# Optimization experiments

Measured on AMD Instinct MI355X. Metric: run time of the kernel, lower is better.

The kernel has to match this reference:

```python
import jax, jax.numpy as jnp
import numpy as np

N_NODES = 50000
N_EDGES = 800000
D = 64
N_GRAPHS = 512
N_LAYERS = 3
HID_FC = 64
N_CLASSES = 10


def setup_inputs() -> dict:
    key = jax.random.key(0)
    ks = jax.random.split(key, 12)
    s = 1.0 / np.sqrt(D)
    x = jax.random.normal(ks[0], (N_NODES, D), dtype=jnp.float32)
    edge_index = jax.random.randint(ks[1], (2, N_EDGES), 0, N_NODES, dtype=jnp.int32)
    batch = jnp.sort(jax.random.randint(ks[2], (N_NODES,), 0, N_GRAPHS, dtype=jnp.int32))
    convW1 = jax.random.normal(ks[3], (N_LAYERS, D, D), dtype=jnp.float32) * s
    convb1 = jax.random.normal(ks[4], (N_LAYERS, D), dtype=jnp.float32) * 0.01
    convW2 = jax.random.normal(ks[5], (N_LAYERS, D, D), dtype=jnp.float32) * s
    convb2 = jax.random.normal(ks[6], (N_LAYERS, D), dtype=jnp.float32) * 0.01
    fcW1 = jax.random.normal(ks[7], (D, HID_FC), dtype=jnp.float32) * s
    fcb1 = jax.random.normal(ks[8], (HID_FC,), dtype=jnp.float32) * 0.01
    fcW2 = jax.random.normal(ks[9], (HID_FC, N_CLASSES), dtype=jnp.float32) * (1.0 / np.sqrt(HID_FC))
    fcb2 = jax.random.normal(ks[10], (N_CLASSES,), dtype=jnp.float32) * 0.01
    return {"x": x, "convW1": convW1, "convb1": convb1, "convW2": convW2,
            "convb2": convb2, "fcW1": fcW1, "fcb1": fcb1, "fcW2": fcW2,
            "fcb2": fcb2, "edge_index": edge_index, "batch": batch}


def reference(x, convW1, convb1, convW2, convb2, fcW1, fcb1, fcW2, fcb2, edge_index, batch):
    src, dst = edge_index[0], edge_index[1]
    h = x
    for l in range(N_LAYERS):
        # GIN aggregation: (1 + eps) * x + sum_{j in N(i)} x_j, eps = 0
        agg = jax.ops.segment_sum(h[src], dst, num_segments=N_NODES)
        h = h + agg
        # per-layer MLP: Linear -> ReLU -> Linear
        h = jax.nn.relu(h @ convW1[l] + convb1[l])
        h = h @ convW2[l] + convb2[l]
    # global max pool over nodes of each graph
    g = jax.ops.segment_max(h, batch, num_segments=N_GRAPHS)
    # FC head: Linear(64) -> ReLU -> Linear(num_classes)
    g = jax.nn.relu(g @ fcW1 + fcb1)
    logits = g @ fcW2 + fcb2
    return jax.nn.log_softmax(logits, axis=1)
```

## Files before the change

kernel.cpp:

```cpp
#include <hip/hip_runtime.h>
#include <math.h>

#define N_NODES 50000
#define N_EDGES 800000
#define D 64
#define N_GRAPHS 512
#define N_CLASSES 10
#define NT 3125
#define NPART 6250

#define SCAN_B 512
#define NB_SCAN ((N_NODES + SCAN_B - 1) / SCAN_B)

typedef __attribute__((ext_vector_type(8))) short bf16x8;
typedef __attribute__((ext_vector_type(4))) float f32x4;

#define MFMA16(a, b, c) __builtin_amdgcn_mfma_f32_16x16x32_bf16(a, b, c, 0, 0, 0)


__device__ __forceinline__ unsigned mapf(float f) {
  unsigned u = __float_as_uint(f);
  return (u & 0x80000000u) ? ~u : (u | 0x80000000u);
}
__device__ __forceinline__ float unmapf(unsigned u) {
  return __uint_as_float((u & 0x80000000u) ? (u & 0x7FFFFFFFu) : ~u);
}
__device__ __forceinline__ ushort bf16_rne(float f) {
  unsigned u = __float_as_uint(f);
  u += 0x7FFFu + ((u >> 16) & 1u);
  return (ushort)(u >> 16);
}
__device__ __forceinline__ float bf16_tof(ushort h) {
  return __uint_as_float(((unsigned)h) << 16);
}
__device__ __forceinline__ unsigned pack2(float a, float b) {
  return (unsigned)bf16_rne(a) | ((unsigned)bf16_rne(b) << 16);
}
__device__ __forceinline__ float2 unpack2(unsigned v) {
  return make_float2(__uint_as_float(v << 16), __uint_as_float(v & 0xFFFF0000u));
}


__global__ void to_bf16(const float* __restrict__ in, unsigned* __restrict__ out) {
  int i = blockIdx.x * 256 + threadIdx.x;
  float4 v = reinterpret_cast<const float4*>(in)[i];
  reinterpret_cast<uint2*>(out)[i] = make_uint2(pack2(v.x, v.y), pack2(v.z, v.w));
}


__global__ void wprep(const float* __restrict__ convW1, const float* __restrict__ convW2,
                      ushort* __restrict__ wf) {
  const int wi = blockIdx.x;
  const int layer = wi >> 1, which = wi & 1;
  const float* W = (which ? convW2 : convW1) + layer * 4096;
  const int t = threadIdx.x;
  const int f = t >> 6, lane = t & 63;
  const int ct = f >> 1, ks = f & 1;
  const int n = ct * 16 + (lane & 15);
  const int k0 = ks * 32 + ((lane >> 4) << 3);
  ushort hi[8], lo[8];
#pragma unroll
  for (int v = 0; v < 8; ++v) {
    float w = W[(k0 + v) * 64 + n];
    ushort h = bf16_rne(w);
    hi[v] = h;
    lo[v] = bf16_rne(w - bf16_tof(h));
  }
  ushort* base = wf + layer * 16384 + which * 8192;
  *(uint4*)(base + f * 512 + lane * 8) = *(uint4*)hi;
  *(uint4*)(base + 4096 + f * 512 + lane * 8) = *(uint4*)lo;
}


__global__ void hist_part(const int* __restrict__ dst, int* __restrict__ deg) {
  const int p = blockIdx.x & 7;
  const int lo = p * NPART, hi = lo + NPART;
  const int stride = (gridDim.x >> 3) * 256;
  for (int e = (blockIdx.x >> 3) * 256 + threadIdx.x; e < N_EDGES; e += stride) {
    int d = dst[e];
    if (d >= lo && d < hi) atomicAdd(&deg[d], 1);
  }
}

__global__ void scan_blocks(const int* __restrict__ deg, int* __restrict__ bsum) {
  __shared__ int sd[SCAN_B];
  int i = blockIdx.x * SCAN_B + threadIdx.x;
  sd[threadIdx.x] = (i < N_NODES) ? deg[i] : 0;
  __syncthreads();
  for (int off = SCAN_B / 2; off > 0; off >>= 1) {
    if (threadIdx.x < off) sd[threadIdx.x] += sd[threadIdx.x + off];
    __syncthreads();
  }
  if (threadIdx.x == 0) bsum[blockIdx.x] = sd[0];
}

__global__ void scan_mid(int* __restrict__ bsum) {
  __shared__ int s[256];
  int t = threadIdx.x;
  if (t < NB_SCAN) s[t] = bsum[t];
  __syncthreads();
  if (t == 0) {
    int run = 0;
    for (int i = 0; i < NB_SCAN; ++i) { int v = s[i]; s[i] = run; run += v; }
  }
  __syncthreads();
  if (t < NB_SCAN) bsum[t] = s[t];
}

__global__ void scan_final(const int* __restrict__ deg, const int* __restrict__ bsum,
                           int* __restrict__ rs, int* __restrict__ cur) {
  __shared__ int sd[SCAN_B];
  int i = blockIdx.x * SCAN_B + threadIdx.x;
  int v = (i < N_NODES) ? deg[i] : 0;
  sd[threadIdx.x] = v;
  __syncthreads();
  for (int off = 1; off < SCAN_B; off <<= 1) {
    int add = (threadIdx.x >= off) ? sd[threadIdx.x - off] : 0;
    __syncthreads();
    sd[threadIdx.x] += add;
    __syncthreads();
  }
  if (i < N_NODES) {
    int ex = bsum[blockIdx.x] + sd[threadIdx.x] - v;
    rs[i] = ex;
    cur[i] = ex;
  }
  if (i == 0) rs[N_NODES] = N_EDGES;
}

__global__ void fill_part(const int* __restrict__ src, const int* __restrict__ dst,
                          int* __restrict__ cur, int* __restrict__ csr) {
  const int p = blockIdx.x & 7;
  const int lo = p * NPART, hi = lo + NPART;
  const int stride = (gridDim.x >> 3) * 256;
  for (int e = (blockIdx.x >> 3) * 256 + threadIdx.x; e < N_EDGES; e += stride) {
    int d = dst[e];
    if (d >= lo && d < hi) {
      int pos = atomicAdd(&cur[d], 1);
      csr[pos] = src[e];
    }
  }
}


__global__ __launch_bounds__(256) void agg_bf16(
    const unsigned* __restrict__ hin, const int* __restrict__ csr,
    const int* __restrict__ rs, unsigned* __restrict__ hout) {
  const int t = threadIdx.x;
  const int hw = t >> 5, hl = t & 31;
  const int node = blockIdx.x * 8 + hw;
  float2 a = unpack2(hin[node * 32 + hl]);
  int e = rs[node];
  const int e1 = rs[node + 1];
  for (; e + 4 <= e1; e += 4) {
    int s0 = csr[e], s1 = csr[e + 1], s2 = csr[e + 2], s3 = csr[e + 3];
    float2 v0 = unpack2(hin[s0 * 32 + hl]);
    float2 v1 = unpack2(hin[s1 * 32 + hl]);
    float2 v2 = unpack2(hin[s2 * 32 + hl]);
    float2 v3 = unpack2(hin[s3 * 32 + hl]);
    a.x += v0.x + v1.x; a.y += v0.y + v1.y;
    a.x += v2.x + v3.x; a.y += v2.y + v3.y;
  }
  for (; e < e1; ++e) {
    float2 v = unpack2(hin[csr[e] * 32 + hl]);
    a.x += v.x; a.y += v.y;
  }
  hout[node * 32 + hl] = pack2(a.x, a.y);
}


template <int FINAL>
__global__ __launch_bounds__(256, 2) void mlp_bf16(
    const unsigned* __restrict__ Ain,
    unsigned* __restrict__ Aout,
    const ushort* __restrict__ wfL,
    const float* __restrict__ b1, const float* __restrict__ b2,
    const int* __restrict__ batch, unsigned* __restrict__ gU) {
  __shared__ ushort Wl[16384];
  __shared__ ushort tb[4][16 * 72];
  const int t = threadIdx.x;
  const int w = t >> 6, lane = t & 63;
  const int tile = blockIdx.x * 4 + w;
  const bool act = (tile < NT);
  const int m = lane & 15, g = lane >> 4;
  ushort* tw = tb[w];

  {
    const uint4* s = (const uint4*)wfL;
    uint4* d = (uint4*)Wl;
#pragma unroll
    for (int i = 0; i < 8; ++i) d[t + 256 * i] = s[t + 256 * i];
  }

  bf16x8 a0 = {}, a1 = {};
  if (act) {
    const ushort* Ar = (const ushort*)Ain + (size_t)(tile * 16 + m) * 64;
    a0 = *(const bf16x8*)(Ar + g * 8);
    a1 = *(const bf16x8*)(Ar + 32 + g * 8);
  }
  __syncthreads();

  const char* wb = (const char*)Wl + lane * 16;
#define LDW(off) (*(const bf16x8*)(wb + (off)))

  if (act) {
    f32x4 c0 = {0.f, 0.f, 0.f, 0.f}, c1 = c0, c2 = c0, c3 = c0;
#define G1(ct, cc)                                        \
    cc = MFMA16(a0, LDW((2 * ct + 0) * 1024), cc);        \
    cc = MFMA16(a1, LDW((2 * ct + 1) * 1024), cc);        \
    cc = MFMA16(a0, LDW(8192 + (2 * ct + 0) * 1024), cc); \
    cc = MFMA16(a1, LDW(8192 + (2 * ct + 1) * 1024), cc);
    G1(0, c0) G1(1, c1) G1(2, c2) G1(3, c3)
#undef G1

    float bv0 = b1[m], bv1 = b1[16 + m], bv2 = b1[32 + m], bv3 = b1[48 + m];
#define WRT(cc, ct, bv)                                                     \
    tw[(g * 4 + 0) * 72 + ct * 16 + m] = bf16_rne(fmaxf(cc[0] + bv, 0.f));  \
    tw[(g * 4 + 1) * 72 + ct * 16 + m] = bf16_rne(fmaxf(cc[1] + bv, 0.f));  \
    tw[(g * 4 + 2) * 72 + ct * 16 + m] = bf16_rne(fmaxf(cc[2] + bv, 0.f));  \
    tw[(g * 4 + 3) * 72 + ct * 16 + m] = bf16_rne(fmaxf(cc[3] + bv, 0.f));
    WRT(c0, 0, bv0) WRT(c1, 1, bv1) WRT(c2, 2, bv2) WRT(c3, 3, bv3)
#undef WRT
    bf16x8 h0 = *(const bf16x8*)(tw + m * 72 + g * 8);
    bf16x8 h1 = *(const bf16x8*)(tw + m * 72 + 32 + g * 8);

    c0 = (f32x4){0.f, 0.f, 0.f, 0.f}; c1 = c0; c2 = c0; c3 = c0;
#define G2(ct, cc)                                         \
    cc = MFMA16(h0, LDW(16384 + (2 * ct + 0) * 1024), cc); \
    cc = MFMA16(h1, LDW(16384 + (2 * ct + 1) * 1024), cc); \
    cc = MFMA16(h0, LDW(24576 + (2 * ct + 0) * 1024), cc); \
    cc = MFMA16(h1, LDW(24576 + (2 * ct + 1) * 1024), cc);
    G2(0, c0) G2(1, c1) G2(2, c2) G2(3, c3)
#undef G2
#undef LDW

    float bv20 = b2[m], bv21 = b2[16 + m], bv22 = b2[32 + m], bv23 = b2[48 + m];
    if (FINAL) {
      int b40 = batch[tile * 16 + g * 4 + 0];
      int b41 = batch[tile * 16 + g * 4 + 1];
      int b42 = batch[tile * 16 + g * 4 + 2];
      int b43 = batch[tile * 16 + g * 4 + 3];
#define PM(cc, ct, bv)                                          \
      atomicMax(&gU[b40 * 64 + ct * 16 + m], mapf(cc[0] + bv)); \
      atomicMax(&gU[b41 * 64 + ct * 16 + m], mapf(cc[1] + bv)); \
      atomicMax(&gU[b42 * 64 + ct * 16 + m], mapf(cc[2] + bv)); \
      atomicMax(&gU[b43 * 64 + ct * 16 + m], mapf(cc[3] + bv));
      PM(c0, 0, bv20) PM(c1, 1, bv21) PM(c2, 2, bv22) PM(c3, 3, bv23)
#undef PM
    } else {
#define WRO(cc, ct, bv)                                          \
      tw[(g * 4 + 0) * 72 + ct * 16 + m] = bf16_rne(cc[0] + bv); \
      tw[(g * 4 + 1) * 72 + ct * 16 + m] = bf16_rne(cc[1] + bv); \
      tw[(g * 4 + 2) * 72 + ct * 16 + m] = bf16_rne(cc[2] + bv); \
      tw[(g * 4 + 3) * 72 + ct * 16 + m] = bf16_rne(cc[3] + bv);
      WRO(c0, 0, bv20) WRO(c1, 1, bv21) WRO(c2, 2, bv22) WRO(c3, 3, bv23)
#undef WRO
      const int r = lane >> 2, q = lane & 3;
      uint4 v0 = *(const uint4*)(tw + r * 72 + q * 16);
      uint4 v1 = *(const uint4*)(tw + r * 72 + q * 16 + 8);
      ushort* Ao = (ushort*)Aout + (size_t)tile * 1024;
      *(uint4*)(Ao + lane * 16) = v0;
      *(uint4*)(Ao + lane * 16 + 8) = v1;
    }
  }
}


__global__ void init_g(unsigned* __restrict__ gU) {
  int i = blockIdx.x * blockDim.x + threadIdx.x;
  if (i < N_GRAPHS * D) gU[i] = 0x007FFFFFu;
}

__global__ void head_kernel(const unsigned* __restrict__ gU,
                            const float* __restrict__ fcW1, const float* __restrict__ fcb1,
                            const float* __restrict__ fcW2, const float* __restrict__ fcb2,
                            float* __restrict__ out) {
  __shared__ float gbuf[64];
  __shared__ float hid[64];
  __shared__ float logit[N_CLASSES];
  __shared__ float red[2];
  const int gi = blockIdx.x;
  const int t = threadIdx.x;

  gbuf[t] = unmapf(gU[gi * D + t]);
  __syncthreads();

  float a = fcb1[t];
#pragma unroll
  for (int k = 0; k < 64; ++k) a = fmaf(gbuf[k], fcW1[k * 64 + t], a);
  hid[t] = fmaxf(a, 0.0f);
  __syncthreads();

  if (t < N_CLASSES) {
    float l = fcb2[t];
#pragma unroll
    for (int k = 0; k < 64; ++k) l = fmaf(hid[k], fcW2[k * N_CLASSES + t], l);
    logit[t] = l;
  }
  __syncthreads();

  if (t == 0) {
    float mx = logit[0];
    for (int i = 1; i < N_CLASSES; ++i) mx = fmaxf(mx, logit[i]);
    float s = 0.0f;
    for (int i = 0; i < N_CLASSES; ++i) s += expf(logit[i] - mx);
    red[0] = mx;
    red[1] = logf(s);
  }
  __syncthreads();

  if (t < N_CLASSES) out[gi * N_CLASSES + t] = logit[t] - red[0] - red[1];
}


extern "C" void kernel_launch(void* const* d_in, const int* in_sizes, int n_in,
                              void* d_out, int out_size, void* d_ws, size_t ws_size,
                              hipStream_t stream) {
  const float* x      = (const float*)d_in[0];
  const float* convW1 = (const float*)d_in[1];
  const float* convb1 = (const float*)d_in[2];
  const float* convW2 = (const float*)d_in[3];
  const float* convb2 = (const float*)d_in[4];
  const float* fcW1   = (const float*)d_in[5];
  const float* fcb1   = (const float*)d_in[6];
  const float* fcW2   = (const float*)d_in[7];
  const float* fcb2   = (const float*)d_in[8];
  const int*   edge   = (const int*)d_in[9];
  const int*   batch  = (const int*)d_in[10];
  float* out = (float*)d_out;

  const int* src = edge;
  const int* dst = edge + N_EDGES;

  unsigned* xb  = (unsigned*)d_ws;
  unsigned* hbA = xb + (size_t)N_NODES * 32;
  unsigned* hbB = hbA + (size_t)N_NODES * 32;
  unsigned* gU  = hbB + (size_t)N_NODES * 32;
  int* rs  = (int*)(gU + N_GRAPHS * D);
  int* csr = rs + N_NODES + 1;
  ushort* wf = (ushort*)(csr + N_EDGES);
  int* deg  = (int*)hbB;
  int* cur  = deg + N_NODES;
  int* bsum = cur + N_NODES;

  to_bf16<<<(N_NODES * 16) / 256, 256, 0, stream>>>(x, xb);
  wprep<<<6, 512, 0, stream>>>(convW1, convW2, wf);
  init_g<<<(N_GRAPHS * D + 255) / 256, 256, 0, stream>>>(gU);

  hipMemsetAsync(deg, 0, N_NODES * sizeof(int), stream);
  hist_part<<<2048, 256, 0, stream>>>(dst, deg);
  scan_blocks<<<NB_SCAN, SCAN_B, 0, stream>>>(deg, bsum);
  scan_mid<<<1, 256, 0, stream>>>(bsum);
  scan_final<<<NB_SCAN, SCAN_B, 0, stream>>>(deg, bsum, rs, cur);
  fill_part<<<2048, 256, 0, stream>>>(src, dst, cur, csr);

  const int AGG_B = N_NODES / 8;
  const int MLP_B = (NT + 3) / 4;
  agg_bf16<<<AGG_B, 256, 0, stream>>>(xb, csr, rs, hbA);
  mlp_bf16<0><<<MLP_B, 256, 0, stream>>>(hbA, hbB, wf, convb1, convb2, batch, gU);
  agg_bf16<<<AGG_B, 256, 0, stream>>>(hbB, csr, rs, hbA);
  mlp_bf16<0><<<MLP_B, 256, 0, stream>>>(hbA, xb, wf + 16384, convb1 + 64, convb2 + 64,
                                         batch, gU);
  agg_bf16<<<AGG_B, 256, 0, stream>>>(xb, csr, rs, hbA);
  mlp_bf16<1><<<MLP_B, 256, 0, stream>>>(hbA, nullptr, wf + 32768, convb1 + 128,
                                         convb2 + 128, batch, gU);

  head_kernel<<<N_GRAPHS, 64, 0, stream>>>(gU, fcW1, fcb1, fcW2, fcb2, out);
}
```

Measured before the change: 228.7 us.

## Make MLP kernel persistent with tile prefetch and amortized weight loads

Launches a fixed 196-block grid for the per-layer MLP kernel, where each wave loops over up to four 16-row tiles. Weights and biases are staged once per block, and the next tile's activations are prefetched while the current tile is computed. The LDS staging row stride changes from 72 to 68 elements, which makes the 16-byte LDS reads misaligned and may alter bank behaviour. It trades grid parallelism for less redundant weight staging and more load overlap.

```diff
diff --git a/kernel.cpp b/kernel.cpp
--- a/kernel.cpp
+++ b/kernel.cpp
@@ -8,6 +8,7 @@
 #define N_CLASSES 10
 #define NT 3125
 #define NPART 6250
+#define MLP_BLOCKS 196
 
 #define SCAN_B 512
 #define NB_SCAN ((N_NODES + SCAN_B - 1) / SCAN_B)
@@ -177,11 +178,9 @@
     const float* __restrict__ b1, const float* __restrict__ b2,
     const int* __restrict__ batch, unsigned* __restrict__ gU) {
   __shared__ ushort Wl[16384];
-  __shared__ ushort tb[4][16 * 72];
+  __shared__ ushort tb[4][16 * 68];
   const int t = threadIdx.x;
   const int w = t >> 6, lane = t & 63;
-  const int tile = blockIdx.x * 4 + w;
-  const bool act = (tile < NT);
   const int m = lane & 15, g = lane >> 4;
   ushort* tw = tb[w];
 
@@ -192,6 +191,8 @@
     for (int i = 0; i < 8; ++i) d[t + 256 * i] = s[t + 256 * i];
   }
 
+  int tile = blockIdx.x * 4 + w;
+  bool act = (tile < NT);
   bf16x8 a0 = {}, a1 = {};
   if (act) {
     const ushort* Ar = (const ushort*)Ain + (size_t)(tile * 16 + m) * 64;
@@ -201,68 +202,83 @@
   __syncthreads();
 
   const char* wb = (const char*)Wl + lane * 16;
+  const float bv10 = b1[m], bv11 = b1[16 + m], bv12 = b1[32 + m], bv13 = b1[48 + m];
+  const float bv20 = b2[m], bv21 = b2[16 + m], bv22 = b2[32 + m], bv23 = b2[48 + m];
+
 #define LDW(off) (*(const bf16x8*)(wb + (off)))
 
-  if (act) {
-    f32x4 c0 = {0.f, 0.f, 0.f, 0.f}, c1 = c0, c2 = c0, c3 = c0;
+#pragma unroll
+  for (int it = 0; it < 4; ++it) {
+    const int ntile = tile + 4 * MLP_BLOCKS;
+    const bool nact = (it < 3) && (ntile < NT);
+    bf16x8 na0 = {}, na1 = {};
+    if (nact) {
+      const ushort* Ar = (const ushort*)Ain + (size_t)(ntile * 16 + m) * 64;
+      na0 = *(const bf16x8*)(Ar + g * 8);
+      na1 = *(const bf16x8*)(Ar + 32 + g * 8);
+    }
+
+    if (act) {
+      f32x4 c0 = {0.f, 0.f, 0.f, 0.f}, c1 = c0, c2 = c0, c3 = c0;
 #define G1(ct, cc)                                        \
-    cc = MFMA16(a0, LDW((2 * ct + 0) * 1024), cc);        \
-    cc = MFMA16(a1, LDW((2 * ct + 1) * 1024), cc);        \
-    cc = MFMA16(a0, LDW(8192 + (2 * ct + 0) * 1024), cc); \
-    cc = MFMA16(a1, LDW(8192 + (2 * ct + 1) * 1024), cc);
-    G1(0, c0) G1(1, c1) G1(2, c2) G1(3, c3)
+      cc = MFMA16(a0, LDW((2 * ct + 0) * 1024), cc);      \
+      cc = MFMA16(a1, LDW((2 * ct + 1) * 1024), cc);      \
+      cc = MFMA16(a0, LDW(8192 + (2 * ct + 0) * 1024), cc); \
+      cc = MFMA16(a1, LDW(8192 + (2 * ct + 1) * 1024), cc);
+      G1(0, c0) G1(1, c1) G1(2, c2) G1(3, c3)
 #undef G1
 
-    float bv0 = b1[m], bv1 = b1[16 + m], bv2 = b1[32 + m], bv3 = b1[48 + m];
 #define WRT(cc, ct, bv)                                                     \
-    tw[(g * 4 + 0) * 72 + ct * 16 + m] = bf16_rne(fmaxf(cc[0] + bv, 0.f));  \
-    tw[(g * 4 + 1) * 72 + ct * 16 + m] = bf16_rne(fmaxf(cc[1] + bv, 0.f));  \
-    tw[(g * 4 + 2) * 72 + ct * 16 + m] = bf16_rne(fmaxf(cc[2] + bv, 0.f));  \
-    tw[(g * 4 + 3) * 72 + ct * 16 + m] = bf16_rne(fmaxf(cc[3] + bv, 0.f));
-    WRT(c0, 0, bv0) WRT(c1, 1, bv1) WRT(c2, 2, bv2) WRT(c3, 3, bv3)
+      tw[(g * 4 + 0) * 68 + ct * 16 + m] = bf16_rne(fmaxf(cc[0] + bv, 0.f)); \
+      tw[(g * 4 + 1) * 68 + ct * 16 + m] = bf16_rne(fmaxf(cc[1] + bv, 0.f)); \
+      tw[(g * 4 + 2) * 68 + ct * 16 + m] = bf16_rne(fmaxf(cc[2] + bv, 0.f)); \
+      tw[(g * 4 + 3) * 68 + ct * 16 + m] = bf16_rne(fmaxf(cc[3] + bv, 0.f));
+      WRT(c0, 0, bv10) WRT(c1, 1, bv11) WRT(c2, 2, bv12) WRT(c3, 3, bv13)
 #undef WRT
-    bf16x8 h0 = *(const bf16x8*)(tw + m * 72 + g * 8);
-    bf16x8 h1 = *(const bf16x8*)(tw + m * 72 + 32 + g * 8);
-
-    c0 = (f32x4){0.f, 0.f, 0.f, 0.f}; c1 = c0; c2 = c0; c3 = c0;
+      bf16x8 h0 = *(const bf16x8*)(tw + m * 68 + g * 8);
+      bf16x8 h1 = *(const bf16x8*)(tw + m * 68 + 32 + g * 8);
+
+      c0 = (f32x4){0.f, 0.f, 0.f, 0.f}; c1 = c0; c2 = c0; c3 = c0;
 #define G2(ct, cc)                                         \
-    cc = MFMA16(h0, LDW(16384 + (2 * ct + 0) * 1024), cc); \
-    cc = MFMA16(h1, LDW(16384 + (2 * ct + 1) * 1024), cc); \
-    cc = MFMA16(h0, LDW(24576 + (2 * ct + 0) * 1024), cc); \
-    cc = MFMA16(h1, LDW(24576 + (2 * ct + 1) * 1024), cc);
-    G2(0, c0) G2(1, c1) G2(2, c2) G2(3, c3)
+      cc = MFMA16(h0, LDW(16384 + (2 * ct + 0) * 1024), cc); \
+      cc = MFMA16(h1, LDW(16384 + (2 * ct + 1) * 1024), cc); \
+      cc = MFMA16(h0, LDW(24576 + (2 * ct + 0) * 1024), cc); \
+      cc = MFMA16(h1, LDW(24576 + (2 * ct + 1) * 1024), cc);
+      G2(0, c0) G2(1, c1) G2(2, c2) G2(3, c3)
 #undef G2
+
+      if (FINAL) {
+        int b40 = batch[tile * 16 + g * 4 + 0];
+        int b41 = batch[tile * 16 + g * 4 + 1];
+        int b42 = batch[tile * 16 + g * 4 + 2];
+        int b43 = batch[tile * 16 + g * 4 + 3];
+#define PM(cc, ct, bv)                                          \
+        atomicMax(&gU[b40 * 64 + ct * 16 + m], mapf(cc[0] + bv)); \
+        atomicMax(&gU[b41 * 64 + ct * 16 + m], mapf(cc[1] + bv)); \
+        atomicMax(&gU[b42 * 64 + ct * 16 + m], mapf(cc[2] + bv)); \
+        atomicMax(&gU[b43 * 64 + ct * 16 + m], mapf(cc[3] + bv));
+        PM(c0, 0, bv20) PM(c1, 1, bv21) PM(c2, 2, bv22) PM(c3, 3, bv23)
+#undef PM
+      } else {
+#define WRO(cc, ct, bv)                                          \
+        tw[(g * 4 + 0) * 68 + ct * 16 + m] = bf16_rne(cc[0] + bv); \
+        tw[(g * 4 + 1) * 68 + ct * 16 + m] = bf16_rne(cc[1] + bv); \
+        tw[(g * 4 + 2) * 68 + ct * 16 + m] = bf16_rne(cc[2] + bv); \
+        tw[(g * 4 + 3) * 68 + ct * 16 + m] = bf16_rne(cc[3] + bv);
+        WRO(c0, 0, bv20) WRO(c1, 1, bv21) WRO(c2, 2, bv22) WRO(c3, 3, bv23)
+#undef WRO
+        const int r = lane >> 2, q = lane & 3;
+        uint4 v0 = *(const uint4*)(tw + r * 68 + q * 16);
+        uint4 v1 = *(const uint4*)(tw + r * 68 + q * 16 + 8);
+        ushort* Ao = (ushort*)Aout + (size_t)tile * 1024;
+        *(uint4*)(Ao + lane * 16) = v0;
+        *(uint4*)(Ao + lane * 16 + 8) = v1;
+      }
+    }
+
+    a0 = na0; a1 = na1; tile = ntile; act = nact;
+  }
 #undef LDW
-
-    float bv20 = b2[m], bv21 = b2[16 + m], bv22 = b2[32 + m], bv23 = b2[48 + m];
-    if (FINAL) {
-      int b40 = batch[tile * 16 + g * 4 + 0];
-      int b41 = batch[tile * 16 + g * 4 + 1];
-      int b42 = batch[tile * 16 + g * 4 + 2];
-      int b43 = batch[tile * 16 + g * 4 + 3];
-#define PM(cc, ct, bv)                                          \
-      atomicMax(&gU[b40 * 64 + ct * 16 + m], mapf(cc[0] + bv)); \
-      atomicMax(&gU[b41 * 64 + ct * 16 + m], mapf(cc[1] + bv)); \
-      atomicMax(&gU[b42 * 64 + ct * 16 + m], mapf(cc[2] + bv)); \
-      atomicMax(&gU[b43 * 64 + ct * 16 + m], mapf(cc[3] + bv));
-      PM(c0, 0, bv20) PM(c1, 1, bv21) PM(c2, 2, bv22) PM(c3, 3, bv23)
-#undef PM
-    } else {
-#define WRO(cc, ct, bv)                                          \
-      tw[(g * 4 + 0) * 72 + ct * 16 + m] = bf16_rne(cc[0] + bv); \
-      tw[(g * 4 + 1) * 72 + ct * 16 + m] = bf16_rne(cc[1] + bv); \
-      tw[(g * 4 + 2) * 72 + ct * 16 + m] = bf16_rne(cc[2] + bv); \
-      tw[(g * 4 + 3) * 72 + ct * 16 + m] = bf16_rne(cc[3] + bv);
-      WRO(c0, 0, bv20) WRO(c1, 1, bv21) WRO(c2, 2, bv22) WRO(c3, 3, bv23)
-#undef WRO
-      const int r = lane >> 2, q = lane & 3;
-      uint4 v0 = *(const uint4*)(tw + r * 72 + q * 16);
-      uint4 v1 = *(const uint4*)(tw + r * 72 + q * 16 + 8);
-      ushort* Ao = (ushort*)Aout + (size_t)tile * 1024;
-      *(uint4*)(Ao + lane * 16) = v0;
-      *(uint4*)(Ao + lane * 16 + 8) = v1;
-    }
-  }
 }
 
 
@@ -355,15 +371,14 @@
   fill_part<<<2048, 256, 0, stream>>>(src, dst, cur, csr);
 
   const int AGG_B = N_NODES / 8;
-  const int MLP_B = (NT + 3) / 4;
   agg_bf16<<<AGG_B, 256, 0, stream>>>(xb, csr, rs, hbA);
-  mlp_bf16<0><<<MLP_B, 256, 0, stream>>>(hbA, hbB, wf, convb1, convb2, batch, gU);
+  mlp_bf16<0><<<MLP_BLOCKS, 256, 0, stream>>>(hbA, hbB, wf, convb1, convb2, batch, gU);
   agg_bf16<<<AGG_B, 256, 0, stream>>>(hbB, csr, rs, hbA);
-  mlp_bf16<0><<<MLP_B, 256, 0, stream>>>(hbA, xb, wf + 16384, convb1 + 64, convb2 + 64,
-                                         batch, gU);
+  mlp_bf16<0><<<MLP_BLOCKS, 256, 0, stream>>>(hbA, xb, wf + 16384, convb1 + 64,
+                                              convb2 + 64, batch, gU);
   agg_bf16<<<AGG_B, 256, 0, stream>>>(xb, csr, rs, hbA);
-  mlp_bf16<1><<<MLP_B, 256, 0, stream>>>(hbA, nullptr, wf + 32768, convb1 + 128,
-                                         convb2 + 128, batch, gU);
+  mlp_bf16<1><<<MLP_BLOCKS, 256, 0, stream>>>(hbA, nullptr, wf + 32768, convb1 + 128,
+                                              convb2 + 128, batch, gU);
 
   head_kernel<<<N_GRAPHS, 64, 0, stream>>>(gU, fcW1, fcb1, fcW2, fcb2, out);
 }
```

After: 233.7 us. +2.2%, slower.

## Fuse neighbor aggregation with per-layer MLP and gather fp32 input directly

Applied to the files above, without the earlier changes.

Merges the separate gather-aggregate and MLP kernels into one per-layer kernel, so each block aggregates 64 nodes into shared memory and runs both MFMA matmuls on them. This removes the bf16 intermediate write/read between aggregation and MLP and three launches. The first layer gathers directly from fp32 x, which drops the to_bf16 conversion kernel but doubles the bytes gathered in that layer. Fewer blocks (782) with a heavier per-block gather phase may reduce latency hiding during the irregular gathers.

```diff
diff --git a/kernel.cpp b/kernel.cpp
--- a/kernel.cpp
+++ b/kernel.cpp
@@ -6,8 +6,8 @@
 #define D 64
 #define N_GRAPHS 512
 #define N_CLASSES 10
-#define NT 3125
 #define NPART 6250
+#define NB_L 782
 
 #define SCAN_B 512
 #define NB_SCAN ((N_NODES + SCAN_B - 1) / SCAN_B)
@@ -38,13 +38,6 @@
 }
 __device__ __forceinline__ float2 unpack2(unsigned v) {
   return make_float2(__uint_as_float(v << 16), __uint_as_float(v & 0xFFFF0000u));
-}
-
-
-__global__ void to_bf16(const float* __restrict__ in, unsigned* __restrict__ out) {
-  int i = blockIdx.x * 256 + threadIdx.x;
-  float4 v = reinterpret_cast<const float4*>(in)[i];
-  reinterpret_cast<uint2*>(out)[i] = make_uint2(pack2(v.x, v.y), pack2(v.z, v.w));
 }
 
 
@@ -143,47 +136,19 @@
 }
 
 
-__global__ __launch_bounds__(256) void agg_bf16(
-    const unsigned* __restrict__ hin, const int* __restrict__ csr,
-    const int* __restrict__ rs, unsigned* __restrict__ hout) {
-  const int t = threadIdx.x;
-  const int hw = t >> 5, hl = t & 31;
-  const int node = blockIdx.x * 8 + hw;
-  float2 a = unpack2(hin[node * 32 + hl]);
-  int e = rs[node];
-  const int e1 = rs[node + 1];
-  for (; e + 4 <= e1; e += 4) {
-    int s0 = csr[e], s1 = csr[e + 1], s2 = csr[e + 2], s3 = csr[e + 3];
-    float2 v0 = unpack2(hin[s0 * 32 + hl]);
-    float2 v1 = unpack2(hin[s1 * 32 + hl]);
-    float2 v2 = unpack2(hin[s2 * 32 + hl]);
-    float2 v3 = unpack2(hin[s3 * 32 + hl]);
-    a.x += v0.x + v1.x; a.y += v0.y + v1.y;
-    a.x += v2.x + v3.x; a.y += v2.y + v3.y;
-  }
-  for (; e < e1; ++e) {
-    float2 v = unpack2(hin[csr[e] * 32 + hl]);
-    a.x += v.x; a.y += v.y;
-  }
-  hout[node * 32 + hl] = pack2(a.x, a.y);
-}
-
-
-template <int FINAL>
-__global__ __launch_bounds__(256, 2) void mlp_bf16(
-    const unsigned* __restrict__ Ain,
-    unsigned* __restrict__ Aout,
+template <int FINAL, int F32IN>
+__global__ __launch_bounds__(256, 3) void gin_layer(
+    const void* __restrict__ hin_, unsigned* __restrict__ hout,
+    const int* __restrict__ csr, const int* __restrict__ rs,
     const ushort* __restrict__ wfL,
     const float* __restrict__ b1, const float* __restrict__ b2,
     const int* __restrict__ batch, unsigned* __restrict__ gU) {
   __shared__ ushort Wl[16384];
-  __shared__ ushort tb[4][16 * 72];
+  __shared__ ushort At[64][72];
   const int t = threadIdx.x;
   const int w = t >> 6, lane = t & 63;
-  const int tile = blockIdx.x * 4 + w;
-  const bool act = (tile < NT);
   const int m = lane & 15, g = lane >> 4;
-  ushort* tw = tb[w];
+  const int base = blockIdx.x * 64;
 
   {
     const uint4* s = (const uint4*)wfL;
@@ -192,73 +157,116 @@
     for (int i = 0; i < 8; ++i) d[t + 256 * i] = s[t + 256 * i];
   }
 
-  bf16x8 a0 = {}, a1 = {};
-  if (act) {
-    const ushort* Ar = (const ushort*)Ain + (size_t)(tile * 16 + m) * 64;
-    a0 = *(const bf16x8*)(Ar + g * 8);
-    a1 = *(const bf16x8*)(Ar + 32 + g * 8);
-  }
-  __syncthreads();
-
+  {
+    const int hw = t >> 5, hl = t & 31;
+    const float* hf = (const float*)hin_;
+    const unsigned* hb = (const unsigned*)hin_;
+    for (int i = 0; i < 8; ++i) {
+      const int nl = hw * 8 + i;
+      const int node = base + nl;
+      float2 a = make_float2(0.f, 0.f);
+      if (node < N_NODES) {
+        if (F32IN) a = ((const float2*)(hf + (size_t)node * 64))[hl];
+        else       a = unpack2(hb[node * 32 + hl]);
+        int e = rs[node];
+        const int e1 = rs[node + 1];
+        if (F32IN) {
+          for (; e + 4 <= e1; e += 4) {
+            int s0 = csr[e], s1 = csr[e + 1], s2 = csr[e + 2], s3 = csr[e + 3];
+            float2 v0 = ((const float2*)(hf + (size_t)s0 * 64))[hl];
+            float2 v1 = ((const float2*)(hf + (size_t)s1 * 64))[hl];
+            float2 v2 = ((const float2*)(hf + (size_t)s2 * 64))[hl];
+            float2 v3 = ((const float2*)(hf + (size_t)s3 * 64))[hl];
+            a.x += v0.x + v1.x; a.y += v0.y + v1.y;
+            a.x += v2.x + v3.x; a.y += v2.y + v3.y;
+          }
+          for (; e < e1; ++e) {
+            float2 v = ((const float2*)(hf + (size_t)csr[e] * 64))[hl];
+            a.x += v.x; a.y += v.y;
+          }
+        } else {
+          for (; e + 4 <= e1; e += 4) {
+            int s0 = csr[e], s1 = csr[e + 1], s2 = csr[e + 2], s3 = csr[e + 3];
+            float2 v0 = unpack2(hb[s0 * 32 + hl]);
+            float2 v1 = unpack2(hb[s1 * 32 + hl]);
+            float2 v2 = unpack2(hb[s2 * 32 + hl]);
+            float2 v3 = unpack2(hb[s3 * 32 + hl]);
+            a.x += v0.x + v1.x; a.y += v0.y + v1.y;
+            a.x += v2.x + v3.x; a.y += v2.y + v3.y;
+          }
+          for (; e < e1; ++e) {
+            float2 v = unpack2(hb[csr[e] * 32 + hl]);
+            a.x += v.x; a.y += v.y;
+          }
+        }
+      }
+      *(unsigned*)&At[nl][2 * hl] = pack2(a.x, a.y);
+    }
+  }
+  __syncthreads();
+
+  bf16x8 a0 = *(const bf16x8*)&At[w * 16 + m][g * 8];
+  bf16x8 a1 = *(const bf16x8*)&At[w * 16 + m][32 + g * 8];
   const char* wb = (const char*)Wl + lane * 16;
+  ushort* tw = &At[w * 16][0];
 #define LDW(off) (*(const bf16x8*)(wb + (off)))
 
-  if (act) {
-    f32x4 c0 = {0.f, 0.f, 0.f, 0.f}, c1 = c0, c2 = c0, c3 = c0;
-#define G1(ct, cc)                                        \
-    cc = MFMA16(a0, LDW((2 * ct + 0) * 1024), cc);        \
-    cc = MFMA16(a1, LDW((2 * ct + 1) * 1024), cc);        \
-    cc = MFMA16(a0, LDW(8192 + (2 * ct + 0) * 1024), cc); \
-    cc = MFMA16(a1, LDW(8192 + (2 * ct + 1) * 1024), cc);
-    G1(0, c0) G1(1, c1) G1(2, c2) G1(3, c3)
+  f32x4 c0 = {0.f, 0.f, 0.f, 0.f}, c1 = c0, c2 = c0, c3 = c0;
+#define G1(ct, cc)                                      \
+  cc = MFMA16(a0, LDW((2 * ct + 0) * 1024), cc);        \
+  cc = MFMA16(a1, LDW((2 * ct + 1) * 1024), cc);        \
+  cc = MFMA16(a0, LDW(8192 + (2 * ct + 0) * 1024), cc); \
+  cc = MFMA16(a1, LDW(8192 + (2 * ct + 1) * 1024), cc);
+  G1(0, c0) G1(1, c1) G1(2, c2) G1(3, c3)
 #undef G1
 
+  {
     float bv0 = b1[m], bv1 = b1[16 + m], bv2 = b1[32 + m], bv3 = b1[48 + m];
-#define WRT(cc, ct, bv)                                                     \
-    tw[(g * 4 + 0) * 72 + ct * 16 + m] = bf16_rne(fmaxf(cc[0] + bv, 0.f));  \
-    tw[(g * 4 + 1) * 72 + ct * 16 + m] = bf16_rne(fmaxf(cc[1] + bv, 0.f));  \
-    tw[(g * 4 + 2) * 72 + ct * 16 + m] = bf16_rne(fmaxf(cc[2] + bv, 0.f));  \
+#define WRT(cc, ct, bv)                                                    \
+    tw[(g * 4 + 0) * 72 + ct * 16 + m] = bf16_rne(fmaxf(cc[0] + bv, 0.f)); \
+    tw[(g * 4 + 1) * 72 + ct * 16 + m] = bf16_rne(fmaxf(cc[1] + bv, 0.f)); \
+    tw[(g * 4 + 2) * 72 + ct * 16 + m] = bf16_rne(fmaxf(cc[2] + bv, 0.f)); \
     tw[(g * 4 + 3) * 72 + ct * 16 + m] = bf16_rne(fmaxf(cc[3] + bv, 0.f));
     WRT(c0, 0, bv0) WRT(c1, 1, bv1) WRT(c2, 2, bv2) WRT(c3, 3, bv3)
 #undef WRT
-    bf16x8 h0 = *(const bf16x8*)(tw + m * 72 + g * 8);
-    bf16x8 h1 = *(const bf16x8*)(tw + m * 72 + 32 + g * 8);
-
-    c0 = (f32x4){0.f, 0.f, 0.f, 0.f}; c1 = c0; c2 = c0; c3 = c0;
-#define G2(ct, cc)                                         \
-    cc = MFMA16(h0, LDW(16384 + (2 * ct + 0) * 1024), cc); \
-    cc = MFMA16(h1, LDW(16384 + (2 * ct + 1) * 1024), cc); \
-    cc = MFMA16(h0, LDW(24576 + (2 * ct + 0) * 1024), cc); \
-    cc = MFMA16(h1, LDW(24576 + (2 * ct + 1) * 1024), cc);
-    G2(0, c0) G2(1, c1) G2(2, c2) G2(3, c3)
+  }
+  bf16x8 h0 = *(const bf16x8*)(tw + m * 72 + g * 8);
+  bf16x8 h1 = *(const bf16x8*)(tw + m * 72 + 32 + g * 8);
+
+  c0 = (f32x4){0.f, 0.f, 0.f, 0.f}; c1 = c0; c2 = c0; c3 = c0;
+#define G2(ct, cc)                                       \
+  cc = MFMA16(h0, LDW(16384 + (2 * ct + 0) * 1024), cc); \
+  cc = MFMA16(h1, LDW(16384 + (2 * ct + 1) * 1024), cc); \
+  cc = MFMA16(h0, LDW(24576 + (2 * ct + 0) * 1024), cc); \
+  cc = MFMA16(h1, LDW(24576 + (2 * ct + 1) * 1024), cc);
+  G2(0, c0) G2(1, c1) G2(2, c2) G2(3, c3)
 #undef G2
 #undef LDW
 
-    float bv20 = b2[m], bv21 = b2[16 + m], bv22 = b2[32 + m], bv23 = b2[48 + m];
-    if (FINAL) {
-      int b40 = batch[tile * 16 + g * 4 + 0];
-      int b41 = batch[tile * 16 + g * 4 + 1];
-      int b42 = batch[tile * 16 + g * 4 + 2];
-      int b43 = batch[tile * 16 + g * 4 + 3];
-#define PM(cc, ct, bv)                                          \
-      atomicMax(&gU[b40 * 64 + ct * 16 + m], mapf(cc[0] + bv)); \
-      atomicMax(&gU[b41 * 64 + ct * 16 + m], mapf(cc[1] + bv)); \
-      atomicMax(&gU[b42 * 64 + ct * 16 + m], mapf(cc[2] + bv)); \
-      atomicMax(&gU[b43 * 64 + ct * 16 + m], mapf(cc[3] + bv));
-      PM(c0, 0, bv20) PM(c1, 1, bv21) PM(c2, 2, bv22) PM(c3, 3, bv23)
+  const float bv20 = b2[m], bv21 = b2[16 + m], bv22 = b2[32 + m], bv23 = b2[48 + m];
+  if (FINAL) {
+    const int tb = base + w * 16;
+#define PM(cc, ct, bv, j)                                             \
+    { int node = tb + g * 4 + j;                                      \
+      if (node < N_NODES)                                             \
+        atomicMax(&gU[batch[node] * 64 + ct * 16 + m], mapf(cc[j] + bv)); }
+#define PM4(cc, ct, bv) PM(cc, ct, bv, 0) PM(cc, ct, bv, 1) PM(cc, ct, bv, 2) PM(cc, ct, bv, 3)
+    PM4(c0, 0, bv20) PM4(c1, 1, bv21) PM4(c2, 2, bv22) PM4(c3, 3, bv23)
+#undef PM4
 #undef PM
-    } else {
-#define WRO(cc, ct, bv)                                          \
-      tw[(g * 4 + 0) * 72 + ct * 16 + m] = bf16_rne(cc[0] + bv); \
-      tw[(g * 4 + 1) * 72 + ct * 16 + m] = bf16_rne(cc[1] + bv); \
-      tw[(g * 4 + 2) * 72 + ct * 16 + m] = bf16_rne(cc[2] + bv); \
-      tw[(g * 4 + 3) * 72 + ct * 16 + m] = bf16_rne(cc[3] + bv);
-      WRO(c0, 0, bv20) WRO(c1, 1, bv21) WRO(c2, 2, bv22) WRO(c3, 3, bv23)
+  } else {
+#define WRO(cc, ct, bv)                                        \
+    tw[(g * 4 + 0) * 72 + ct * 16 + m] = bf16_rne(cc[0] + bv); \
+    tw[(g * 4 + 1) * 72 + ct * 16 + m] = bf16_rne(cc[1] + bv); \
+    tw[(g * 4 + 2) * 72 + ct * 16 + m] = bf16_rne(cc[2] + bv); \
+    tw[(g * 4 + 3) * 72 + ct * 16 + m] = bf16_rne(cc[3] + bv);
+    WRO(c0, 0, bv20) WRO(c1, 1, bv21) WRO(c2, 2, bv22) WRO(c3, 3, bv23)
 #undef WRO
-      const int r = lane >> 2, q = lane & 3;
+    const int r = lane >> 2, q = lane & 3;
+    if (base + w * 16 + r < N_NODES) {
       uint4 v0 = *(const uint4*)(tw + r * 72 + q * 16);
       uint4 v1 = *(const uint4*)(tw + r * 72 + q * 16 + 8);
-      ushort* Ao = (ushort*)Aout + (size_t)tile * 1024;
+      ushort* Ao = (ushort*)hout + (size_t)(base + w * 16) * 64;
       *(uint4*)(Ao + lane * 16) = v0;
       *(uint4*)(Ao + lane * 16 + 8) = v1;
     }
@@ -332,18 +340,16 @@
   const int* src = edge;
   const int* dst = edge + N_EDGES;
 
-  unsigned* xb  = (unsigned*)d_ws;
-  unsigned* hbA = xb + (size_t)N_NODES * 32;
+  unsigned* hbA = (unsigned*)d_ws;
   unsigned* hbB = hbA + (size_t)N_NODES * 32;
   unsigned* gU  = hbB + (size_t)N_NODES * 32;
   int* rs  = (int*)(gU + N_GRAPHS * D);
   int* csr = rs + N_NODES + 1;
   ushort* wf = (ushort*)(csr + N_EDGES);
-  int* deg  = (int*)hbB;
+  int* deg  = (int*)hbA;
   int* cur  = deg + N_NODES;
   int* bsum = cur + N_NODES;
 
-  to_bf16<<<(N_NODES * 16) / 256, 256, 0, stream>>>(x, xb);
   wprep<<<6, 512, 0, stream>>>(convW1, convW2, wf);
   init_g<<<(N_GRAPHS * D + 255) / 256, 256, 0, stream>>>(gU);
 
@@ -354,16 +360,12 @@
   scan_final<<<NB_SCAN, SCAN_B, 0, stream>>>(deg, bsum, rs, cur);
   fill_part<<<2048, 256, 0, stream>>>(src, dst, cur, csr);
 
-  const int AGG_B = N_NODES / 8;
-  const int MLP_B = (NT + 3) / 4;
-  agg_bf16<<<AGG_B, 256, 0, stream>>>(xb, csr, rs, hbA);
-  mlp_bf16<0><<<MLP_B, 256, 0, stream>>>(hbA, hbB, wf, convb1, convb2, batch, gU);
-  agg_bf16<<<AGG_B, 256, 0, stream>>>(hbB, csr, rs, hbA);
-  mlp_bf16<0><<<MLP_B, 256, 0, stream>>>(hbA, xb, wf + 16384, convb1 + 64, convb2 + 64,
-                                         batch, gU);
-  agg_bf16<<<AGG_B, 256, 0, stream>>>(xb, csr, rs, hbA);
-  mlp_bf16<1><<<MLP_B, 256, 0, stream>>>(hbA, nullptr, wf + 32768, convb1 + 128,
-                                         convb2 + 128, batch, gU);
+  gin_layer<0, 1><<<NB_L, 256, 0, stream>>>(x, hbA, csr, rs, wf,
+                                            convb1, convb2, batch, gU);
+  gin_layer<0, 0><<<NB_L, 256, 0, stream>>>(hbA, hbB, csr, rs, wf + 16384,
+                                            convb1 + 64, convb2 + 64, batch, gU);
+  gin_layer<1, 0><<<NB_L, 256, 0, stream>>>(hbB, nullptr, csr, rs, wf + 32768,
+                                            convb1 + 128, convb2 + 128, batch, gU);
 
   head_kernel<<<N_GRAPHS, 64, 0, stream>>>(gU, fcW1, fcb1, fcW2, fcb2, out);
 }
```

New measurement: 338.4 us. +47.9%, slower.
